# Kernel tuning notes

Hardware: AMD Instinct MI355X
Metric: run time of the kernel (lower is better)

## Reference

```python
import jax, jax.numpy as jnp
import numpy as np

LN_EPS = 1e-5
LEAKY_SLOPE = 0.01


def setup_inputs() -> dict:
    key = jax.random.key(0)
    k1, k2, k3 = jax.random.split(key, 3)
    n, d, ns = 200000, 512, 1024
    x = jax.random.normal(k1, (n, d), dtype=jnp.float32)
    # Kaiming-ish scale for the projection weight [3d, d]
    W = jax.random.normal(k2, (3 * d, d), dtype=jnp.float32) * (1.0 / np.sqrt(3 * d))
    b = jnp.zeros((d,), dtype=jnp.float32)
    gamma = jnp.ones((d,), dtype=jnp.float32)
    beta = jnp.zeros((d,), dtype=jnp.float32)
    batch = jnp.sort(jax.random.randint(k3, (n,), 0, ns, dtype=jnp.int32))
    return {"x": x, "W": W, "b": b, "gamma": gamma, "beta": beta,
            "batch": batch, "num_segments": ns}


def _pool_mean_max_std(x, batch, num_segments):
    # single-pass style segment reductions: sum, sum-of-squares, count, max
    n = x.shape[0]
    count = jax.ops.segment_sum(jnp.ones((n,), x.dtype), batch, num_segments)  # [S]
    s = jax.ops.segment_sum(x, batch, num_segments)                            # [S,d]
    sq = jax.ops.segment_sum(x * x, batch, num_segments)                       # [S,d]
    cnt = jnp.maximum(count, 1.0)[:, None]
    mean = s / cnt                                                             # global_mean_pool
    # masked dense amax == segment max; empty segments -> finfo.min (NEG fill)
    NEG = jnp.finfo(x.dtype).min
    xmax = jax.ops.segment_max(x, batch, num_segments)
    xmax = jnp.where(jnp.isfinite(xmax), xmax, NEG)
    # scatter_std, unbiased=True, divisor clamped to >= 1 (torch_scatter semantics)
    var = (sq - mean * s) / jnp.maximum(count - 1.0, 1.0)[:, None]
    var = jnp.maximum(var, 0.0)
    safe = jnp.where(var > 0, var, 1.0)
    std = jnp.where(var > 0, jnp.sqrt(safe), 0.0)
    return jnp.concatenate([mean, xmax, std], axis=-1)  # [S, 3d]


def reference(x, W, b, gamma, beta, batch, num_segments):
    pooled = _pool_mean_max_std(x, batch, num_segments)        # [S, 3d]
    h = pooled @ W + b                                          # Linear
    mu = jnp.mean(h, axis=-1, keepdims=True)                    # LayerNorm (eps=1e-5)
    v = jnp.mean((h - mu) ** 2, axis=-1, keepdims=True)
    h = (h - mu) / jnp.sqrt(v + LN_EPS) * gamma + beta
    return jnp.where(h >= 0, h, LEAKY_SLOPE * h)                # LeakyReLU
```

## Files before the change

kernel.cpp:

```cpp
#include <hip/hip_runtime.h>
#include <math.h>

#define D 512
#define K3D 1536
#define NEGF (-3.40282346638528859812e+38f)

__device__ __forceinline__ int lower_bound_dev(const int* __restrict__ b, int n, int v) {
    int lo = 0, hi = n;
    while (lo < hi) {
        int mid = (lo + hi) >> 1;
        if (b[mid] < v) lo = mid + 1; else hi = mid;
    }
    return lo;
}

__device__ __forceinline__ void acc4(float4& s, float4& q, float4& m, const float4 v) {
    s.x += v.x; s.y += v.y; s.z += v.z; s.w += v.w;
    q.x = fmaf(v.x, v.x, q.x); q.y = fmaf(v.y, v.y, q.y);
    q.z = fmaf(v.z, v.z, q.z); q.w = fmaf(v.w, v.w, q.w);
    m.x = fmaxf(m.x, v.x); m.y = fmaxf(m.y, v.y);
    m.z = fmaxf(m.z, v.z); m.w = fmaxf(m.w, v.w);
}

__global__ __launch_bounds__(256) void pool_kernel(
    const float* __restrict__ x, const int* __restrict__ batch,
    float* __restrict__ pooled, int n) {
    const int s   = blockIdx.x;
    const int col = threadIdx.x & 127;
    const int rw  = threadIdx.x >> 7;
    const int start = lower_bound_dev(batch, n, s);
    const int end   = lower_bound_dev(batch, n, s + 1);

    const float4* __restrict__ xv = (const float4*)x;

    float4 sum = {0.f, 0.f, 0.f, 0.f};
    float4 sq  = {0.f, 0.f, 0.f, 0.f};
    float4 mx  = {-INFINITY, -INFINITY, -INFINITY, -INFINITY};

    int i = start + rw;
    for (; i + 6 < end; i += 8) {
        float4 v0 = xv[(size_t)(i + 0) * 128 + col];
        float4 v1 = xv[(size_t)(i + 2) * 128 + col];
        float4 v2 = xv[(size_t)(i + 4) * 128 + col];
        float4 v3 = xv[(size_t)(i + 6) * 128 + col];
        acc4(sum, sq, mx, v0);
        acc4(sum, sq, mx, v1);
        acc4(sum, sq, mx, v2);
        acc4(sum, sq, mx, v3);
    }
    for (; i < end; i += 2) {
        float4 v0 = xv[(size_t)i * 128 + col];
        acc4(sum, sq, mx, v0);
    }

    __shared__ __align__(16) float4 red[3 * 128];
    if (rw == 1) {
        red[col]       = sum;
        red[128 + col] = sq;
        red[256 + col] = mx;
    }
    __syncthreads();
    if (rw == 0) {
        float4 s2 = red[col], q2 = red[128 + col], m2 = red[256 + col];
        sum.x += s2.x; sum.y += s2.y; sum.z += s2.z; sum.w += s2.w;
        sq.x  += q2.x; sq.y  += q2.y; sq.z  += q2.z; sq.w  += q2.w;
        mx.x = fmaxf(mx.x, m2.x); mx.y = fmaxf(mx.y, m2.y);
        mx.z = fmaxf(mx.z, m2.z); mx.w = fmaxf(mx.w, m2.w);

        const float cnt  = (float)(end - start);
        const float inv  = 1.f / fmaxf(cnt, 1.f);
        const float dinv = 1.f / fmaxf(cnt - 1.f, 1.f);

        float4 mean, stdv, mxo;
        mean.x = sum.x * inv; mean.y = sum.y * inv;
        mean.z = sum.z * inv; mean.w = sum.w * inv;

        float vx = (sq.x - mean.x * sum.x) * dinv;
        float vy = (sq.y - mean.y * sum.y) * dinv;
        float vz = (sq.z - mean.z * sum.z) * dinv;
        float vw = (sq.w - mean.w * sum.w) * dinv;
        vx = fmaxf(vx, 0.f); vy = fmaxf(vy, 0.f);
        vz = fmaxf(vz, 0.f); vw = fmaxf(vw, 0.f);
        stdv.x = vx > 0.f ? sqrtf(vx) : 0.f;
        stdv.y = vy > 0.f ? sqrtf(vy) : 0.f;
        stdv.z = vz > 0.f ? sqrtf(vz) : 0.f;
        stdv.w = vw > 0.f ? sqrtf(vw) : 0.f;

        mxo.x = isfinite(mx.x) ? mx.x : NEGF;
        mxo.y = isfinite(mx.y) ? mx.y : NEGF;
        mxo.z = isfinite(mx.z) ? mx.z : NEGF;
        mxo.w = isfinite(mx.w) ? mx.w : NEGF;

        float4* prow = (float4*)(pooled + (size_t)s * K3D);
        prow[col]       = mean;
        prow[128 + col] = mxo;
        prow[256 + col] = stdv;
    }
}

#define BM 32
#define BN 64
#define BK 32
#define LDA 36
#define SPLITK 4
#define KCHUNK (K3D / SPLITK)

__global__ __launch_bounds__(128) void gemm_kernel(
    const float* __restrict__ A, const float* __restrict__ W,
    float* __restrict__ Hp, int S) {
    __shared__ __align__(16) float AsT[BK * LDA];
    __shared__ __align__(16) float Bs[BK * BN];

    const int tid = threadIdx.x;
    const int m0 = blockIdx.y * BM;
    const int j0 = blockIdx.x * BN;
    const int kb = blockIdx.z * KCHUNK;
    const int tr = tid >> 4;
    const int tc = tid & 15;

    const int kq = tid & 7;
    const int am = tid >> 3;
    const int jq = tid & 15;
    const int kr = tid >> 4;

    float acc[4][4] = {};

    for (int k0 = kb; k0 < kb + KCHUNK; k0 += BK) {
        float4 a0 = *(const float4*)&A[(size_t)(m0 + am)      * K3D + k0 + 4 * kq];
        float4 a1 = *(const float4*)&A[(size_t)(m0 + am + 16) * K3D + k0 + 4 * kq];
        float4 b0 = *(const float4*)&W[(size_t)(k0 + kr)      * D + j0 + 4 * jq];
        float4 b1 = *(const float4*)&W[(size_t)(k0 + kr +  8) * D + j0 + 4 * jq];
        float4 b2 = *(const float4*)&W[(size_t)(k0 + kr + 16) * D + j0 + 4 * jq];
        float4 b3 = *(const float4*)&W[(size_t)(k0 + kr + 24) * D + j0 + 4 * jq];

        __syncthreads();
        AsT[(4 * kq + 0) * LDA + am] = a0.x;
        AsT[(4 * kq + 1) * LDA + am] = a0.y;
        AsT[(4 * kq + 2) * LDA + am] = a0.z;
        AsT[(4 * kq + 3) * LDA + am] = a0.w;
        AsT[(4 * kq + 0) * LDA + am + 16] = a1.x;
        AsT[(4 * kq + 1) * LDA + am + 16] = a1.y;
        AsT[(4 * kq + 2) * LDA + am + 16] = a1.z;
        AsT[(4 * kq + 3) * LDA + am + 16] = a1.w;
        *(float4*)&Bs[(kr)      * BN + 4 * jq] = b0;
        *(float4*)&Bs[(kr +  8) * BN + 4 * jq] = b1;
        *(float4*)&Bs[(kr + 16) * BN + 4 * jq] = b2;
        *(float4*)&Bs[(kr + 24) * BN + 4 * jq] = b3;
        __syncthreads();

#pragma unroll
        for (int kk = 0; kk < BK; ++kk) {
            float4 av = *(const float4*)&AsT[kk * LDA + 4 * tr];
            float4 bv = *(const float4*)&Bs[kk * BN + 4 * tc];
            acc[0][0] = fmaf(av.x, bv.x, acc[0][0]);
            acc[0][1] = fmaf(av.x, bv.y, acc[0][1]);
            acc[0][2] = fmaf(av.x, bv.z, acc[0][2]);
            acc[0][3] = fmaf(av.x, bv.w, acc[0][3]);
            acc[1][0] = fmaf(av.y, bv.x, acc[1][0]);
            acc[1][1] = fmaf(av.y, bv.y, acc[1][1]);
            acc[1][2] = fmaf(av.y, bv.z, acc[1][2]);
            acc[1][3] = fmaf(av.y, bv.w, acc[1][3]);
            acc[2][0] = fmaf(av.z, bv.x, acc[2][0]);
            acc[2][1] = fmaf(av.z, bv.y, acc[2][1]);
            acc[2][2] = fmaf(av.z, bv.z, acc[2][2]);
            acc[2][3] = fmaf(av.z, bv.w, acc[2][3]);
            acc[3][0] = fmaf(av.w, bv.x, acc[3][0]);
            acc[3][1] = fmaf(av.w, bv.y, acc[3][1]);
            acc[3][2] = fmaf(av.w, bv.z, acc[3][2]);
            acc[3][3] = fmaf(av.w, bv.w, acc[3][3]);
        }
    }

    float* out = Hp + (size_t)blockIdx.z * S * D;
#pragma unroll
    for (int i = 0; i < 4; ++i) {
        float4 o = {acc[i][0], acc[i][1], acc[i][2], acc[i][3]};
        *(float4*)&out[(size_t)(m0 + 4 * tr + i) * D + j0 + 4 * tc] = o;
    }
}

__global__ __launch_bounds__(128) void ln_kernel(
    const float* __restrict__ Hp, const float* __restrict__ bias,
    const float* __restrict__ gamma, const float* __restrict__ beta,
    float* __restrict__ out, int S) {
    const int row = blockIdx.x;
    const int tid = threadIdx.x;
    const size_t idx = (size_t)row * 128 + tid;
    const size_t stride = (size_t)S * 128;

    const float4* hp = (const float4*)Hp;
    float4 v0 = hp[idx];
    float4 v1 = hp[idx + stride];
    float4 v2 = hp[idx + 2 * stride];
    float4 v3 = hp[idx + 3 * stride];
    float4 bb = *(const float4*)&bias[4 * tid];
    float4 v;
    v.x = v0.x + v1.x + v2.x + v3.x + bb.x;
    v.y = v0.y + v1.y + v2.y + v3.y + bb.y;
    v.z = v0.z + v1.z + v2.z + v3.z + bb.z;
    v.w = v0.w + v1.w + v2.w + v3.w + bb.w;

    float s = v.x + v.y + v.z + v.w;
    float q = v.x * v.x + v.y * v.y + v.z * v.z + v.w * v.w;
#pragma unroll
    for (int off = 32; off > 0; off >>= 1) {
        s += __shfl_down(s, off);
        q += __shfl_down(q, off);
    }
    __shared__ float ls[2], lq[2];
    const int wave = tid >> 6, lane = tid & 63;
    if (lane == 0) { ls[wave] = s; lq[wave] = q; }
    __syncthreads();
    s = ls[0] + ls[1];
    q = lq[0] + lq[1];

    const float mu = s * (1.f / 512.f);
    float var = q * (1.f / 512.f) - mu * mu;
    var = fmaxf(var, 0.f);
    const float r = rsqrtf(var + 1e-5f);

    float4 g  = *(const float4*)&gamma[4 * tid];
    float4 bt = *(const float4*)&beta[4 * tid];
    float4 o;
    o.x = (v.x - mu) * r * g.x + bt.x;
    o.y = (v.y - mu) * r * g.y + bt.y;
    o.z = (v.z - mu) * r * g.z + bt.z;
    o.w = (v.w - mu) * r * g.w + bt.w;
    o.x = o.x >= 0.f ? o.x : 0.01f * o.x;
    o.y = o.y >= 0.f ? o.y : 0.01f * o.y;
    o.z = o.z >= 0.f ? o.z : 0.01f * o.z;
    o.w = o.w >= 0.f ? o.w : 0.01f * o.w;
    *(float4*)&out[(size_t)row * D + 4 * tid] = o;
}

extern "C" void kernel_launch(void* const* d_in, const int* in_sizes, int n_in,
                              void* d_out, int out_size, void* d_ws, size_t ws_size,
                              hipStream_t stream) {
    const float* x     = (const float*)d_in[0];
    const float* W     = (const float*)d_in[1];
    const float* b     = (const float*)d_in[2];
    const float* gamma = (const float*)d_in[3];
    const float* beta  = (const float*)d_in[4];
    const int*   batch = (const int*)d_in[5];
    const int n = in_sizes[5];
    const int S = out_size / D;

    float* pooled = (float*)d_ws;
    float* Hp     = pooled + (size_t)S * K3D;
    float* out    = (float*)d_out;

    pool_kernel<<<S, 256, 0, stream>>>(x, batch, pooled, n);
    dim3 g2(D / BN, S / BM, SPLITK);
    gemm_kernel<<<g2, 128, 0, stream>>>(pooled, W, Hp, S);
    ln_kernel<<<S, 128, 0, stream>>>(Hp, b, gamma, beta, out, S);
}
```

Measured before the change: 583.1 us.

## Switch projection GEMM to bf16 MFMA with bf16 pooled output and transposed weights

The pooling kernel now writes its pooled features as bf16. A new kernel transposes W and converts it to bf16. The fp32 FMA GEMM is replaced by an MFMA 16x16x32 bf16 kernel with 64x64x64 tiles and 4-way split-K. The aim is to move the GEMM onto matrix cores and halve the operand traffic, at the cost of bf16 rounding on the pooled and weight operands and one extra launch per call.

Result: faster. 563.4 us (-3.4%).

```diff
diff --git a/kernel.cpp b/kernel.cpp
--- a/kernel.cpp
+++ b/kernel.cpp
@@ -4,6 +4,16 @@
 #define D 512
 #define K3D 1536
 #define NEGF (-3.40282346638528859812e+38f)
+
+typedef __bf16 bf16x8 __attribute__((ext_vector_type(8)));
+typedef unsigned short ushort8v __attribute__((ext_vector_type(8)));
+typedef float f32x4 __attribute__((ext_vector_type(4)));
+
+__device__ __forceinline__ unsigned short f2bf(float f) {
+    unsigned int u = __float_as_uint(f);
+    unsigned int r = (u + 0x7FFFu + ((u >> 16) & 1u)) >> 16;
+    return (unsigned short)r;
+}
 
 __device__ __forceinline__ int lower_bound_dev(const int* __restrict__ b, int n, int v) {
     int lo = 0, hi = n;
@@ -24,7 +34,7 @@
 
 __global__ __launch_bounds__(256) void pool_kernel(
     const float* __restrict__ x, const int* __restrict__ batch,
-    float* __restrict__ pooled, int n) {
+    unsigned short* __restrict__ pooled_b, int n) {
     const int s   = blockIdx.x;
     const int col = threadIdx.x & 127;
     const int rw  = threadIdx.x >> 7;
@@ -71,7 +81,7 @@
         const float inv  = 1.f / fmaxf(cnt, 1.f);
         const float dinv = 1.f / fmaxf(cnt - 1.f, 1.f);
 
-        float4 mean, stdv, mxo;
+        float4 mean, stdv;
         mean.x = sum.x * inv; mean.y = sum.y * inv;
         mean.z = sum.z * inv; mean.w = sum.w * inv;
 
@@ -86,96 +96,106 @@
         stdv.z = vz > 0.f ? sqrtf(vz) : 0.f;
         stdv.w = vw > 0.f ? sqrtf(vw) : 0.f;
 
-        mxo.x = isfinite(mx.x) ? mx.x : NEGF;
-        mxo.y = isfinite(mx.y) ? mx.y : NEGF;
-        mxo.z = isfinite(mx.z) ? mx.z : NEGF;
-        mxo.w = isfinite(mx.w) ? mx.w : NEGF;
-
-        float4* prow = (float4*)(pooled + (size_t)s * K3D);
-        prow[col]       = mean;
-        prow[128 + col] = mxo;
-        prow[256 + col] = stdv;
-    }
-}
-
-#define BM 32
-#define BN 64
-#define BK 32
-#define LDA 36
-#define SPLITK 4
-#define KCHUNK (K3D / SPLITK)
-
-__global__ __launch_bounds__(128) void gemm_kernel(
-    const float* __restrict__ A, const float* __restrict__ W,
+        float mxx = isfinite(mx.x) ? mx.x : NEGF;
+        float mxy = isfinite(mx.y) ? mx.y : NEGF;
+        float mxz = isfinite(mx.z) ? mx.z : NEGF;
+        float mxw = isfinite(mx.w) ? mx.w : NEGF;
+
+        unsigned short* prow = pooled_b + (size_t)s * K3D;
+        ushort4 om = { f2bf(mean.x), f2bf(mean.y), f2bf(mean.z), f2bf(mean.w) };
+        ushort4 ox = { f2bf(mxx),    f2bf(mxy),    f2bf(mxz),    f2bf(mxw)    };
+        ushort4 os = { f2bf(stdv.x), f2bf(stdv.y), f2bf(stdv.z), f2bf(stdv.w) };
+        *(ushort4*)&prow[4 * col]        = om;
+        *(ushort4*)&prow[512 + 4 * col]  = ox;
+        *(ushort4*)&prow[1024 + 4 * col] = os;
+    }
+}
+
+__global__ __launch_bounds__(256) void wconv_kernel(
+    const float* __restrict__ W, unsigned short* __restrict__ Wt) {
+    __shared__ float tile[32][33];
+    const int c0 = blockIdx.x * 32;
+    const int r0 = blockIdx.y * 32;
+    const int t = threadIdx.x;
+    const int r = t >> 3, c4 = (t & 7) * 4;
+    float4 v = *(const float4*)&W[(size_t)(r0 + r) * D + c0 + c4];
+    tile[r][c4 + 0] = v.x; tile[r][c4 + 1] = v.y;
+    tile[r][c4 + 2] = v.z; tile[r][c4 + 3] = v.w;
+    __syncthreads();
+    const int nn = t >> 3, k4 = (t & 7) * 4;
+    ushort4 o = { f2bf(tile[k4 + 0][nn]), f2bf(tile[k4 + 1][nn]),
+                  f2bf(tile[k4 + 2][nn]), f2bf(tile[k4 + 3][nn]) };
+    *(ushort4*)&Wt[(size_t)(c0 + nn) * K3D + r0 + k4] = o;
+}
+
+#define GBM 64
+#define GBN 64
+#define GBK 64
+#define LDT 88
+#define GSPLIT 4
+#define GKC (K3D / GSPLIT)
+
+__global__ __launch_bounds__(256) void mfma_gemm(
+    const unsigned short* __restrict__ A,
+    const unsigned short* __restrict__ B,
     float* __restrict__ Hp, int S) {
-    __shared__ __align__(16) float AsT[BK * LDA];
-    __shared__ __align__(16) float Bs[BK * BN];
-
-    const int tid = threadIdx.x;
-    const int m0 = blockIdx.y * BM;
-    const int j0 = blockIdx.x * BN;
-    const int kb = blockIdx.z * KCHUNK;
-    const int tr = tid >> 4;
-    const int tc = tid & 15;
-
-    const int kq = tid & 7;
-    const int am = tid >> 3;
-    const int jq = tid & 15;
-    const int kr = tid >> 4;
-
-    float acc[4][4] = {};
-
-    for (int k0 = kb; k0 < kb + KCHUNK; k0 += BK) {
-        float4 a0 = *(const float4*)&A[(size_t)(m0 + am)      * K3D + k0 + 4 * kq];
-        float4 a1 = *(const float4*)&A[(size_t)(m0 + am + 16) * K3D + k0 + 4 * kq];
-        float4 b0 = *(const float4*)&W[(size_t)(k0 + kr)      * D + j0 + 4 * jq];
-        float4 b1 = *(const float4*)&W[(size_t)(k0 + kr +  8) * D + j0 + 4 * jq];
-        float4 b2 = *(const float4*)&W[(size_t)(k0 + kr + 16) * D + j0 + 4 * jq];
-        float4 b3 = *(const float4*)&W[(size_t)(k0 + kr + 24) * D + j0 + 4 * jq];
-
+    __shared__ unsigned short As[GBM * LDT];
+    __shared__ unsigned short Bs[GBN * LDT];
+
+    const int tid  = threadIdx.x;
+    const int wave = tid >> 6;
+    const int lane = tid & 63;
+    const int m0 = blockIdx.y * GBM;
+    const int n0 = blockIdx.x * GBN;
+    const int kb = blockIdx.z * GKC;
+    const int wm = (wave & 1) * 32;
+    const int wn = (wave >> 1) * 32;
+
+    const int sr = tid >> 3;
+    const int sc = (tid & 7) * 8;
+
+    const int frow = lane & 15;
+    const int fk   = (lane >> 4) * 8;
+
+    f32x4 acc00 = {0.f, 0.f, 0.f, 0.f};
+    f32x4 acc01 = {0.f, 0.f, 0.f, 0.f};
+    f32x4 acc10 = {0.f, 0.f, 0.f, 0.f};
+    f32x4 acc11 = {0.f, 0.f, 0.f, 0.f};
+
+    for (int k0 = kb; k0 < kb + GKC; k0 += GBK) {
+        ushort8v a0 = *(const ushort8v*)&A[(size_t)(m0 + sr)      * K3D + k0 + sc];
+        ushort8v a1 = *(const ushort8v*)&A[(size_t)(m0 + sr + 32) * K3D + k0 + sc];
+        ushort8v b0 = *(const ushort8v*)&B[(size_t)(n0 + sr)      * K3D + k0 + sc];
+        ushort8v b1 = *(const ushort8v*)&B[(size_t)(n0 + sr + 32) * K3D + k0 + sc];
         __syncthreads();
-        AsT[(4 * kq + 0) * LDA + am] = a0.x;
-        AsT[(4 * kq + 1) * LDA + am] = a0.y;
-        AsT[(4 * kq + 2) * LDA + am] = a0.z;
-        AsT[(4 * kq + 3) * LDA + am] = a0.w;
-        AsT[(4 * kq + 0) * LDA + am + 16] = a1.x;
-        AsT[(4 * kq + 1) * LDA + am + 16] = a1.y;
-        AsT[(4 * kq + 2) * LDA + am + 16] = a1.z;
-        AsT[(4 * kq + 3) * LDA + am + 16] = a1.w;
-        *(float4*)&Bs[(kr)      * BN + 4 * jq] = b0;
-        *(float4*)&Bs[(kr +  8) * BN + 4 * jq] = b1;
-        *(float4*)&Bs[(kr + 16) * BN + 4 * jq] = b2;
-        *(float4*)&Bs[(kr + 24) * BN + 4 * jq] = b3;
+        *(ushort8v*)&As[(sr)      * LDT + sc] = a0;
+        *(ushort8v*)&As[(sr + 32) * LDT + sc] = a1;
+        *(ushort8v*)&Bs[(sr)      * LDT + sc] = b0;
+        *(ushort8v*)&Bs[(sr + 32) * LDT + sc] = b1;
         __syncthreads();
 
 #pragma unroll
-        for (int kk = 0; kk < BK; ++kk) {
-            float4 av = *(const float4*)&AsT[kk * LDA + 4 * tr];
-            float4 bv = *(const float4*)&Bs[kk * BN + 4 * tc];
-            acc[0][0] = fmaf(av.x, bv.x, acc[0][0]);
-            acc[0][1] = fmaf(av.x, bv.y, acc[0][1]);
-            acc[0][2] = fmaf(av.x, bv.z, acc[0][2]);
-            acc[0][3] = fmaf(av.x, bv.w, acc[0][3]);
-            acc[1][0] = fmaf(av.y, bv.x, acc[1][0]);
-            acc[1][1] = fmaf(av.y, bv.y, acc[1][1]);
-            acc[1][2] = fmaf(av.y, bv.z, acc[1][2]);
-            acc[1][3] = fmaf(av.y, bv.w, acc[1][3]);
-            acc[2][0] = fmaf(av.z, bv.x, acc[2][0]);
-            acc[2][1] = fmaf(av.z, bv.y, acc[2][1]);
-            acc[2][2] = fmaf(av.z, bv.z, acc[2][2]);
-            acc[2][3] = fmaf(av.z, bv.w, acc[2][3]);
-            acc[3][0] = fmaf(av.w, bv.x, acc[3][0]);
-            acc[3][1] = fmaf(av.w, bv.y, acc[3][1]);
-            acc[3][2] = fmaf(av.w, bv.z, acc[3][2]);
-            acc[3][3] = fmaf(av.w, bv.w, acc[3][3]);
+        for (int ks = 0; ks < GBK; ks += 32) {
+            bf16x8 af0 = *(const bf16x8*)&As[(wm + frow)      * LDT + ks + fk];
+            bf16x8 af1 = *(const bf16x8*)&As[(wm + 16 + frow) * LDT + ks + fk];
+            bf16x8 bv0 = *(const bf16x8*)&Bs[(wn + frow)      * LDT + ks + fk];
+            bf16x8 bv1 = *(const bf16x8*)&Bs[(wn + 16 + frow) * LDT + ks + fk];
+            acc00 = __builtin_amdgcn_mfma_f32_16x16x32_bf16(af0, bv0, acc00, 0, 0, 0);
+            acc01 = __builtin_amdgcn_mfma_f32_16x16x32_bf16(af0, bv1, acc01, 0, 0, 0);
+            acc10 = __builtin_amdgcn_mfma_f32_16x16x32_bf16(af1, bv0, acc10, 0, 0, 0);
+            acc11 = __builtin_amdgcn_mfma_f32_16x16x32_bf16(af1, bv1, acc11, 0, 0, 0);
         }
     }
 
     float* out = Hp + (size_t)blockIdx.z * S * D;
+    const int orow = (lane >> 4) * 4;
+    const int ocol = lane & 15;
 #pragma unroll
-    for (int i = 0; i < 4; ++i) {
-        float4 o = {acc[i][0], acc[i][1], acc[i][2], acc[i][3]};
-        *(float4*)&out[(size_t)(m0 + 4 * tr + i) * D + j0 + 4 * tc] = o;
+    for (int r = 0; r < 4; ++r) {
+        out[(size_t)(m0 + wm +      orow + r) * D + n0 + wn +      ocol] = acc00[r];
+        out[(size_t)(m0 + wm +      orow + r) * D + n0 + wn + 16 + ocol] = acc01[r];
+        out[(size_t)(m0 + wm + 16 + orow + r) * D + n0 + wn +      ocol] = acc10[r];
+        out[(size_t)(m0 + wm + 16 + orow + r) * D + n0 + wn + 16 + ocol] = acc11[r];
     }
 }
 
@@ -195,10 +215,10 @@
     float4 v3 = hp[idx + 3 * stride];
     float4 bb = *(const float4*)&bias[4 * tid];
     float4 v;
-    v.x = v0.x + v1.x + v2.x + v3.x + bb.x;
-    v.y = v0.y + v1.y + v2.y + v3.y + bb.y;
-    v.z = v0.z + v1.z + v2.z + v3.z + bb.z;
-    v.w = v0.w + v1.w + v2.w + v3.w + bb.w;
+    v.x = (v0.x + v1.x) + (v2.x + v3.x) + bb.x;
+    v.y = (v0.y + v1.y) + (v2.y + v3.y) + bb.y;
+    v.z = (v0.z + v1.z) + (v2.z + v3.z) + bb.z;
+    v.w = (v0.w + v1.w) + (v2.w + v3.w) + bb.w;
 
     float s = v.x + v.y + v.z + v.w;
     float q = v.x * v.x + v.y * v.y + v.z * v.z + v.w * v.w;
@@ -245,12 +265,16 @@
     const int n = in_sizes[5];
     const int S = out_size / D;
 
-    float* pooled = (float*)d_ws;
-    float* Hp     = pooled + (size_t)S * K3D;
-    float* out    = (float*)d_out;
-
-    pool_kernel<<<S, 256, 0, stream>>>(x, batch, pooled, n);
-    dim3 g2(D / BN, S / BM, SPLITK);
-    gemm_kernel<<<g2, 128, 0, stream>>>(pooled, W, Hp, S);
+    char* ws = (char*)d_ws;
+    unsigned short* pooled_b = (unsigned short*)ws;
+    unsigned short* Wt       = (unsigned short*)(ws + (size_t)S * K3D * 2);
+    float*          Hp       = (float*)(ws + (size_t)S * K3D * 2 + (size_t)D * K3D * 2);
+    float* out = (float*)d_out;
+
+    pool_kernel<<<S, 256, 0, stream>>>(x, batch, pooled_b, n);
+    dim3 gw(D / 32, K3D / 32);
+    wconv_kernel<<<gw, 256, 0, stream>>>(W, Wt);
+    dim3 gg(D / GBN, S / GBM, GSPLIT);
+    mfma_gemm<<<gg, 256, 0, stream>>>(pooled_b, Wt, Hp, S);
     ln_kernel<<<S, 128, 0, stream>>>(Hp, b, gamma, beta, out, S);
 }
```
